# Performance work log

Hardware: AMD Instinct MI355X
Metric: run time of the kernel (lower is better)

The kernel has to match this reference:

```python
import jax, jax.numpy as jnp
import numpy as np

B = 4096       # batch
S = 4096       # seq_len == input_dim
DEPTH = 2
D_MODEL = 1
D_FFN = 2      # d_model * d_ffn_factor
EPS = 1e-5


def _layernorm(x, w, b):
    mu = jnp.mean(x, axis=-1, keepdims=True)
    var = jnp.mean((x - mu) ** 2, axis=-1, keepdims=True)
    return (x - mu) * jax.lax.rsqrt(var + EPS) * w + b


def setup_inputs() -> dict:
    key = jax.random.key(0)
    ks = jax.random.split(key, 16)
    sc = lambda fan_in: 1.0 / np.sqrt(fan_in)
    inp = {
        "x": jax.random.normal(ks[0], (B, S), dtype=jnp.float32),
        # per-depth stacked gMLP block params
        "ln1_w": jnp.ones((DEPTH, D_MODEL), jnp.float32),
        "ln1_b": jnp.zeros((DEPTH, D_MODEL), jnp.float32),
        "cp1_w": jax.random.uniform(ks[1], (DEPTH, D_FFN, D_MODEL), jnp.float32, -sc(D_MODEL), sc(D_MODEL)),
        "cp1_b": jax.random.uniform(ks[2], (DEPTH, D_FFN), jnp.float32, -sc(D_MODEL), sc(D_MODEL)),
        "sgu_ln_w": jnp.ones((DEPTH, D_FFN // 2), jnp.float32),
        "sgu_ln_b": jnp.zeros((DEPTH, D_FFN // 2), jnp.float32),
        "sgu_proj_w": jax.random.uniform(ks[3], (DEPTH, S, S), jnp.float32, -sc(S), sc(S)),
        "sgu_proj_b": jax.random.uniform(ks[4], (DEPTH, S), jnp.float32, -sc(S), sc(S)),
        "cp2_w": jax.random.uniform(ks[5], (DEPTH, D_MODEL, D_FFN // 2), jnp.float32, -sc(D_FFN // 2), sc(D_FFN // 2)),
        "cp2_b": jax.random.uniform(ks[6], (DEPTH, D_MODEL), jnp.float32, -sc(D_FFN // 2), sc(D_FFN // 2)),
        "pooler_w": jax.random.uniform(ks[7], (S, S), jnp.float32, -sc(S), sc(S)),
        "pooler_b": jax.random.uniform(ks[8], (S,), jnp.float32, -sc(S), sc(S)),
        "cls_w": jax.random.uniform(ks[9], (1, S), jnp.float32, -sc(S), sc(S)),
        "cls_b": jax.random.uniform(ks[10], (1,), jnp.float32, -sc(S), sc(S)),
    }
    return inp


def reference(x, ln1_w, ln1_b, cp1_w, cp1_b, sgu_ln_w, sgu_ln_b,
              sgu_proj_w, sgu_proj_b, cp2_w, cp2_b,
              pooler_w, pooler_b, cls_w, cls_b):
    gelu = lambda t: jax.nn.gelu(t, approximate=False)
    h = x[..., None]                                   # [B, S, 1]
    for i in range(DEPTH):
        res = h
        t = _layernorm(h, ln1_w[i], ln1_b[i])          # [B, S, 1]
        t = gelu(t @ cp1_w[i].T + cp1_b[i])            # [B, S, 2]
        u, v = t[..., :D_FFN // 2], t[..., D_FFN // 2:]
        v = _layernorm(v, sgu_ln_w[i], sgu_ln_b[i])
        # transpose(1,2) -> Linear(S,S) -> transpose back, fused as einsum
        v = jnp.einsum('st,btc->bsc', sgu_proj_w[i], v) + sgu_proj_b[i][:, None]
        h = u * v                                      # [B, S, 1]
        h = h @ cp2_w[i].T + cp2_b[i] + res            # [B, S, 1]
    out = h[..., 0]                                    # [B, S]
    out = gelu(out @ pooler_w.T + pooler_b)            # [B, S]
    logits = out @ cls_w.T + cls_b                     # [B, 1]
    return logits[..., 0]                              # [B]
```

## Files before the change

kernel.cpp:

```cpp
#include <hip/hip_runtime.h>


#define K_DIM 4096

typedef __bf16 bf16x8 __attribute__((ext_vector_type(8)));
typedef float f32x4 __attribute__((ext_vector_type(4)));

__device__ __forceinline__ ushort f2bf(float f) {
    unsigned int u = __float_as_uint(f);
    u = (u + 0x7fffu + ((u >> 16) & 1u)) >> 16;
    return (ushort)u;
}

__device__ __forceinline__ float gelu_exact(float x) {
    return 0.5f * x * (1.0f + erff(x * 0.70710678118654752440f));
}

__device__ __forceinline__ void gld16(const void* g, void* l) {
    __builtin_amdgcn_global_load_lds(
        (__attribute__((address_space(1))) void*)(g),
        (__attribute__((address_space(3))) void*)(l), 16, 0, 0);
}

__global__ __launch_bounds__(256) void c_kernel(const float* __restrict__ ln1_b,
                                                const float* __restrict__ cp1_w,
                                                const float* __restrict__ cp1_b,
                                                const float* __restrict__ sgu_ln_b,
                                                const float* __restrict__ sgu_proj_w,
                                                const float* __restrict__ sgu_proj_b,
                                                const float* __restrict__ cp2_w,
                                                const float* __restrict__ cp2_b,
                                                const float* __restrict__ cls_b,
                                                const float* __restrict__ pooler_b,
                                                float* __restrict__ c,
                                                float* __restrict__ e,
                                                float* __restrict__ out) {
    int t = blockIdx.x * 256 + threadIdx.x;
    float cv = 0.0f;
#pragma unroll
    for (int i = 0; i < 2; ++i) {
        float alpha = gelu_exact(ln1_b[i] * cp1_w[i * 2 + 0] + cp1_b[i * 2 + 0]);
        float beta  = sgu_ln_b[i];
        float Ri = 0.0f;
        if (beta != 0.0f) {
            const float* pr = sgu_proj_w + ((size_t)i * 4096 + t) * K_DIM;
            for (int k = 0; k < K_DIM; k += 4) {
                float4 pv = *(const float4*)&pr[k];
                Ri += pv.x + pv.y + pv.z + pv.w;
            }
        }
        float v = beta * Ri + sgu_proj_b[i * 4096 + t];
        cv += alpha * v * cp2_w[i] + cp2_b[i];
    }
    c[t]   = cv;
    e[t]   = pooler_b[t];
    out[t] = cls_b[0];
}

__global__ __launch_bounds__(256) void cvt2_kernel(const float* __restrict__ s0,
                                                   ushort* __restrict__ d0,
                                                   const float* __restrict__ s1,
                                                   ushort* __restrict__ d1,
                                                   const float* __restrict__ c,
                                                   float* __restrict__ e) {
    int b = blockIdx.x;
    bool isP = (b >= 8192);
    const float* src = isP ? s1 : s0;
    ushort* dst = isP ? d1 : d0;
    int i = (b & 8191) * 256 + threadIdx.x;
    const float4* s4 = (const float4*)src + (size_t)i * 2;
    float4 a = s4[0], q = s4[1];
    union { ushort u[8]; uint4 v; } r;
    r.u[0] = f2bf(a.x); r.u[1] = f2bf(a.y); r.u[2] = f2bf(a.z); r.u[3] = f2bf(a.w);
    r.u[4] = f2bf(q.x); r.u[5] = f2bf(q.y); r.u[6] = f2bf(q.z); r.u[7] = f2bf(q.w);
    ((uint4*)dst)[i] = r.v;
    if (isP) {
        int col = (i << 3) & 4095;
        float s = a.x * c[col + 0] + a.y * c[col + 1] + a.z * c[col + 2] + a.w * c[col + 3]
                + q.x * c[col + 4] + q.y * c[col + 5] + q.z * c[col + 6] + q.w * c[col + 7];
#pragma unroll
        for (int m = 1; m < 64; m <<= 1) s += __shfl_xor(s, m);
        if ((threadIdx.x & 63) == 0) atomicAdd(&e[i >> 9], s);
    }
}

__global__ __launch_bounds__(512, 2) void gemm_kernel(const ushort* __restrict__ X,
                                                      const ushort* __restrict__ P,
                                                      const float* __restrict__ clsW,
                                                      const float* __restrict__ e,
                                                      float* __restrict__ accOut) {
    __shared__ __align__(16) ushort As[2][256 * 64];
    __shared__ __align__(16) ushort Bs[2][256 * 64];

    const int t = threadIdx.x;
    const int flat = blockIdx.x;
    const int swz = (flat & 7) * 32 + (flat >> 3);
    const int bRow = swz >> 4, bCol = swz & 15;

    const int lane = t & 63, wv = t >> 6;
    const int g = lane >> 4, lo = lane & 15;
    const int wm = wv >> 2, wn = wv & 3;

    f32x4 zero4 = {0.f, 0.f, 0.f, 0.f};
    f32x4 acc[8][4];
#pragma unroll
    for (int mi = 0; mi < 8; ++mi)
#pragma unroll
        for (int ni = 0; ni < 4; ++ni) acc[mi][ni] = zero4;

    const int sr2 = t >> 3;
    const int cs = (t & 7) ^ (sr2 & 7);
    const ushort* gA = X + (size_t)(bRow * 256 + sr2) * K_DIM + cs * 8;
    const ushort* gB = P + (size_t)(bCol * 256 + sr2) * K_DIM + cs * 8;
    char* lA0 = (char*)&As[0][0] + t * 16;
    char* lB0 = (char*)&Bs[0][0] + t * 16;

#define STAGE_A(buf, h, k0)                                                        \
    do {                                                                           \
        gld16(gA + (size_t)((h) * 128) * K_DIM + (k0), lA0 + (buf) * 32768 + (h) * 16384);      \
        gld16(gA + (size_t)((h) * 128 + 64) * K_DIM + (k0), lA0 + (buf) * 32768 + (h) * 16384 + 8192); \
    } while (0)
#define STAGE_B(buf, h, k0)                                                        \
    do {                                                                           \
        gld16(gB + (size_t)((h) * 128) * K_DIM + (k0), lB0 + (buf) * 32768 + (h) * 16384);      \
        gld16(gB + (size_t)((h) * 128 + 64) * K_DIM + (k0), lB0 + (buf) * 32768 + (h) * 16384 + 8192); \
    } while (0)

#define VMW4 asm volatile("s_waitcnt vmcnt(4)" ::: "memory")
#define VMW0 asm volatile("s_waitcnt vmcnt(0)" ::: "memory")
#define NOSTAGE ((void)0)
#define NOWAIT ((void)0)

#define PHASE(buf, qm, qn, STG, WAIT)                                              \
    do {                                                                           \
        bf16x8 af[4][2], bfr[2][2];                                                \
        _Pragma("unroll") for (int m_ = 0; m_ < 4; ++m_)                           \
            _Pragma("unroll") for (int kk_ = 0; kk_ < 2; ++kk_)                    \
                af[m_][kk_] = *(const bf16x8*)&As[buf][((qm) * 128 + wm * 64 + m_ * 16 + lo) * 64 + ((((kk_ << 2) | g) ^ (lo & 7)) << 3)]; \
        _Pragma("unroll") for (int n_ = 0; n_ < 2; ++n_)                           \
            _Pragma("unroll") for (int kk_ = 0; kk_ < 2; ++kk_)                    \
                bfr[n_][kk_] = *(const bf16x8*)&Bs[buf][((qn) * 128 + wn * 32 + n_ * 16 + lo) * 64 + ((((kk_ << 2) | g) ^ (lo & 7)) << 3)]; \
        STG;                                                                       \
        __builtin_amdgcn_s_barrier();                                              \
        asm volatile("s_waitcnt lgkmcnt(0)" ::: "memory");                         \
        __builtin_amdgcn_sched_barrier(0);                                         \
        __builtin_amdgcn_s_setprio(1);                                             \
        _Pragma("unroll") for (int m_ = 0; m_ < 4; ++m_)                           \
            _Pragma("unroll") for (int n_ = 0; n_ < 2; ++n_)                       \
                _Pragma("unroll") for (int kk_ = 0; kk_ < 2; ++kk_)                \
                    acc[(qm) * 4 + m_][(qn) * 2 + n_] = __builtin_amdgcn_mfma_f32_16x16x32_bf16( \
                        af[m_][kk_], bfr[n_][kk_], acc[(qm) * 4 + m_][(qn) * 2 + n_], 0, 0, 0); \
        __builtin_amdgcn_s_setprio(0);                                             \
        WAIT;                                                                      \
        __builtin_amdgcn_s_barrier();                                              \
    } while (0)

    STAGE_A(0, 0, 0);  STAGE_B(0, 0, 0);
    STAGE_A(0, 1, 0);  STAGE_B(0, 1, 0);
    STAGE_A(1, 0, 64); STAGE_B(1, 0, 64);
    VMW4;
    __builtin_amdgcn_s_barrier();

#pragma unroll 1
    for (int k0 = 0; k0 < 3968; k0 += 128) {
        PHASE(0, 0, 0, STAGE_A(1, 1, k0 + 64),  NOWAIT);
        PHASE(0, 0, 1, STAGE_B(1, 1, k0 + 64),  NOWAIT);
        PHASE(0, 1, 0, STAGE_A(0, 0, k0 + 128), NOWAIT);
        PHASE(0, 1, 1, STAGE_B(0, 0, k0 + 128), VMW4);
        PHASE(1, 0, 0, STAGE_A(0, 1, k0 + 128), NOWAIT);
        PHASE(1, 0, 1, STAGE_B(0, 1, k0 + 128), NOWAIT);
        PHASE(1, 1, 0, STAGE_A(1, 0, k0 + 192), NOWAIT);
        PHASE(1, 1, 1, STAGE_B(1, 0, k0 + 192), VMW4);
    }
    PHASE(0, 0, 0, STAGE_A(1, 1, 4032), NOWAIT);
    PHASE(0, 0, 1, STAGE_B(1, 1, 4032), NOWAIT);
    PHASE(0, 1, 0, NOSTAGE, NOWAIT);
    PHASE(0, 1, 1, NOSTAGE, VMW0);
    PHASE(1, 0, 0, NOSTAGE, NOWAIT);
    PHASE(1, 0, 1, NOSTAGE, NOWAIT);
    PHASE(1, 1, 0, NOSTAGE, NOWAIT);
    PHASE(1, 1, 1, NOSTAGE, NOWAIT);

#undef PHASE
#undef STAGE_A
#undef STAGE_B

    float eb[4], cw[4];
#pragma unroll
    for (int ni = 0; ni < 4; ++ni) {
        int s = bCol * 256 + (ni >> 1) * 128 + wn * 32 + (ni & 1) * 16 + lo;
        eb[ni] = e[s];
        cw[ni] = clsW[s];
    }
#pragma unroll
    for (int mi = 0; mi < 8; ++mi) {
        int rowBase = bRow * 256 + (mi >> 2) * 128 + wm * 64 + (mi & 3) * 16 + g * 4;
#pragma unroll
        for (int r = 0; r < 4; ++r) {
            float sum = 0.0f;
#pragma unroll
            for (int ni = 0; ni < 4; ++ni) {
                float y = acc[mi][ni][r] + eb[ni];
                sum += gelu_exact(y) * cw[ni];
            }
            sum += __shfl_xor(sum, 1);
            sum += __shfl_xor(sum, 2);
            sum += __shfl_xor(sum, 4);
            sum += __shfl_xor(sum, 8);
            if (lo == 0) atomicAdd(&accOut[rowBase + r], sum);
        }
    }
}

extern "C" void kernel_launch(void* const* d_in, const int* in_sizes, int n_in,
                              void* d_out, int out_size, void* d_ws, size_t ws_size,
                              hipStream_t stream) {
    const float* x          = (const float*)d_in[0];
    const float* ln1_b      = (const float*)d_in[2];
    const float* cp1_w      = (const float*)d_in[3];
    const float* cp1_b      = (const float*)d_in[4];
    const float* sgu_ln_b   = (const float*)d_in[6];
    const float* sgu_proj_w = (const float*)d_in[7];
    const float* sgu_proj_b = (const float*)d_in[8];
    const float* cp2_w      = (const float*)d_in[9];
    const float* cp2_b      = (const float*)d_in[10];
    const float* pooler_w   = (const float*)d_in[11];
    const float* pooler_b   = (const float*)d_in[12];
    const float* cls_w      = (const float*)d_in[13];
    const float* cls_b      = (const float*)d_in[14];

    ushort* xb = (ushort*)d_ws;
    ushort* pb = xb + (size_t)K_DIM * K_DIM;
    float*  fs = (float*)(pb + (size_t)K_DIM * K_DIM);
    float* c_buf = fs;
    float* e_buf = fs + 4096;
    float* out   = (float*)d_out;

    c_kernel<<<16, 256, 0, stream>>>(ln1_b, cp1_w, cp1_b, sgu_ln_b, sgu_proj_w,
                                     sgu_proj_b, cp2_w, cp2_b, cls_b, pooler_b,
                                     c_buf, e_buf, out);
    cvt2_kernel<<<16384, 256, 0, stream>>>(x, xb, pooler_w, pb, c_buf, e_buf);
    gemm_kernel<<<256, 512, 0, stream>>>(xb, pb, cls_w, e_buf, out);
}
```

Baseline: 429.8 us.

## Reuse register fragments across GEMM phases and deepen global prefetch

The main GEMM loop now keeps A/B fragments in registers shared across the four quadrant phases, ordered (0,0)->(1,0)->(1,1)->(0,1). Each phase reloads only the operand that changes, which cuts LDS reads per k-step. Global-to-LDS staging is reordered to keep one more stage in flight (vmcnt 6 instead of 4), and the first phase waits with a partial lgkmcnt. This adds register pressure and more complex buffer-hazard reasoning in exchange for less LDS traffic and more load latency hiding.

```diff
diff --git a/kernel.cpp b/kernel.cpp
--- a/kernel.cpp
+++ b/kernel.cpp
@@ -108,6 +108,11 @@
 #pragma unroll
         for (int ni = 0; ni < 4; ++ni) acc[mi][ni] = zero4;
 
+    bf16x8 af[4][2];
+    bf16x8 bfr[2][2];
+    const int ch0 = ((g ^ (lo & 7)) << 3);
+    const int ch1 = (((4 | g) ^ (lo & 7)) << 3);
+
     const int sr2 = t >> 3;
     const int cs = (t & 7) ^ (sr2 & 7);
     const ushort* gA = X + (size_t)(bRow * 256 + sr2) * K_DIM + cs * 8;
@@ -126,62 +131,82 @@
         gld16(gB + (size_t)((h) * 128 + 64) * K_DIM + (k0), lB0 + (buf) * 32768 + (h) * 16384 + 8192); \
     } while (0)
 
-#define VMW4 asm volatile("s_waitcnt vmcnt(4)" ::: "memory")
+#define VMW6 asm volatile("s_waitcnt vmcnt(6)" ::: "memory")
 #define VMW0 asm volatile("s_waitcnt vmcnt(0)" ::: "memory")
 #define NOSTAGE ((void)0)
 #define NOWAIT ((void)0)
-
-#define PHASE(buf, qm, qn, STG, WAIT)                                              \
-    do {                                                                           \
-        bf16x8 af[4][2], bfr[2][2];                                                \
-        _Pragma("unroll") for (int m_ = 0; m_ < 4; ++m_)                           \
-            _Pragma("unroll") for (int kk_ = 0; kk_ < 2; ++kk_)                    \
-                af[m_][kk_] = *(const bf16x8*)&As[buf][((qm) * 128 + wm * 64 + m_ * 16 + lo) * 64 + ((((kk_ << 2) | g) ^ (lo & 7)) << 3)]; \
-        _Pragma("unroll") for (int n_ = 0; n_ < 2; ++n_)                           \
-            _Pragma("unroll") for (int kk_ = 0; kk_ < 2; ++kk_)                    \
-                bfr[n_][kk_] = *(const bf16x8*)&Bs[buf][((qn) * 128 + wn * 32 + n_ * 16 + lo) * 64 + ((((kk_ << 2) | g) ^ (lo & 7)) << 3)]; \
-        STG;                                                                       \
-        __builtin_amdgcn_s_barrier();                                              \
-        asm volatile("s_waitcnt lgkmcnt(0)" ::: "memory");                         \
-        __builtin_amdgcn_sched_barrier(0);                                         \
+#define BAR __builtin_amdgcn_s_barrier()
+#define LGKM0                                                \
+    do {                                                     \
+        asm volatile("s_waitcnt lgkmcnt(0)" ::: "memory");   \
+        __builtin_amdgcn_sched_barrier(0);                   \
+    } while (0)
+
+#define READ_A(buf, qm)                                                            \
+    _Pragma("unroll") for (int m_ = 0; m_ < 4; ++m_) {                             \
+        af[m_][0] = *(const bf16x8*)&As[buf][((qm) * 128 + wm * 64 + m_ * 16 + lo) * 64 + ch0]; \
+        af[m_][1] = *(const bf16x8*)&As[buf][((qm) * 128 + wm * 64 + m_ * 16 + lo) * 64 + ch1]; \
+    }
+#define READ_B(buf, qn)                                                            \
+    _Pragma("unroll") for (int n_ = 0; n_ < 2; ++n_) {                             \
+        bfr[n_][0] = *(const bf16x8*)&Bs[buf][((qn) * 128 + wn * 32 + n_ * 16 + lo) * 64 + ch0]; \
+        bfr[n_][1] = *(const bf16x8*)&Bs[buf][((qn) * 128 + wn * 32 + n_ * 16 + lo) * 64 + ch1]; \
+    }
+#define MFMA16(qm, qn)                                                             \
+    do {                                                                           \
         __builtin_amdgcn_s_setprio(1);                                             \
         _Pragma("unroll") for (int m_ = 0; m_ < 4; ++m_)                           \
-            _Pragma("unroll") for (int n_ = 0; n_ < 2; ++n_)                       \
-                _Pragma("unroll") for (int kk_ = 0; kk_ < 2; ++kk_)                \
-                    acc[(qm) * 4 + m_][(qn) * 2 + n_] = __builtin_amdgcn_mfma_f32_16x16x32_bf16( \
-                        af[m_][kk_], bfr[n_][kk_], acc[(qm) * 4 + m_][(qn) * 2 + n_], 0, 0, 0); \
+            _Pragma("unroll") for (int n_ = 0; n_ < 2; ++n_) {                     \
+                acc[(qm) * 4 + m_][(qn) * 2 + n_] = __builtin_amdgcn_mfma_f32_16x16x32_bf16( \
+                    af[m_][0], bfr[n_][0], acc[(qm) * 4 + m_][(qn) * 2 + n_], 0, 0, 0); \
+                acc[(qm) * 4 + m_][(qn) * 2 + n_] = __builtin_amdgcn_mfma_f32_16x16x32_bf16( \
+                    af[m_][1], bfr[n_][1], acc[(qm) * 4 + m_][(qn) * 2 + n_], 0, 0, 0); \
+            }                                                                      \
         __builtin_amdgcn_s_setprio(0);                                             \
-        WAIT;                                                                      \
-        __builtin_amdgcn_s_barrier();                                              \
-    } while (0)
-
-    STAGE_A(0, 0, 0);  STAGE_B(0, 0, 0);
-    STAGE_A(0, 1, 0);  STAGE_B(0, 1, 0);
-    STAGE_A(1, 0, 64); STAGE_B(1, 0, 64);
-    VMW4;
-    __builtin_amdgcn_s_barrier();
+    } while (0)
+
+#define PH1(b, STG)                                                                \
+    do {                                                                           \
+        READ_A(b, 0); READ_B(b, 0); STG;                                           \
+        asm volatile("s_waitcnt lgkmcnt(8)" ::: "memory");                         \
+        BAR; LGKM0; MFMA16(0, 0); BAR;                                             \
+    } while (0)
+#define PH2(b, STG) do { READ_A(b, 1); STG; BAR; LGKM0; MFMA16(1, 0); BAR; } while (0)
+#define PH3(b, STG) do { READ_B(b, 1); STG; BAR; LGKM0; MFMA16(1, 1); BAR; } while (0)
+#define PH4(b, STG, WAIT) do { READ_A(b, 0); STG; BAR; LGKM0; MFMA16(0, 1); WAIT; BAR; } while (0)
+
+    STAGE_B(0, 0, 0);  STAGE_A(0, 1, 0);  STAGE_B(0, 1, 0);  STAGE_A(0, 0, 0);
+    STAGE_B(1, 0, 64); STAGE_A(1, 1, 64); STAGE_B(1, 1, 64);
+    VMW6;
+    BAR;
 
 #pragma unroll 1
     for (int k0 = 0; k0 < 3968; k0 += 128) {
-        PHASE(0, 0, 0, STAGE_A(1, 1, k0 + 64),  NOWAIT);
-        PHASE(0, 0, 1, STAGE_B(1, 1, k0 + 64),  NOWAIT);
-        PHASE(0, 1, 0, STAGE_A(0, 0, k0 + 128), NOWAIT);
-        PHASE(0, 1, 1, STAGE_B(0, 0, k0 + 128), VMW4);
-        PHASE(1, 0, 0, STAGE_A(0, 1, k0 + 128), NOWAIT);
-        PHASE(1, 0, 1, STAGE_B(0, 1, k0 + 128), NOWAIT);
-        PHASE(1, 1, 0, STAGE_A(1, 0, k0 + 192), NOWAIT);
-        PHASE(1, 1, 1, STAGE_B(1, 0, k0 + 192), VMW4);
-    }
-    PHASE(0, 0, 0, STAGE_A(1, 1, 4032), NOWAIT);
-    PHASE(0, 0, 1, STAGE_B(1, 1, 4032), NOWAIT);
-    PHASE(0, 1, 0, NOSTAGE, NOWAIT);
-    PHASE(0, 1, 1, NOSTAGE, VMW0);
-    PHASE(1, 0, 0, NOSTAGE, NOWAIT);
-    PHASE(1, 0, 1, NOSTAGE, NOWAIT);
-    PHASE(1, 1, 0, NOSTAGE, NOWAIT);
-    PHASE(1, 1, 1, NOSTAGE, NOWAIT);
-
-#undef PHASE
+        PH1(0, STAGE_A(1, 0, k0 + 64));
+        PH2(0, STAGE_B(0, 0, k0 + 128));
+        PH3(0, STAGE_A(0, 1, k0 + 128));
+        PH4(0, STAGE_B(0, 1, k0 + 128), VMW6);
+        PH1(1, STAGE_A(0, 0, k0 + 128));
+        PH2(1, STAGE_B(1, 0, k0 + 192));
+        PH3(1, STAGE_A(1, 1, k0 + 192));
+        PH4(1, STAGE_B(1, 1, k0 + 192), VMW6);
+    }
+    PH1(0, STAGE_A(1, 0, 4032));
+    PH2(0, NOSTAGE);
+    PH3(0, NOSTAGE);
+    PH4(0, NOSTAGE, VMW0);
+    PH1(1, NOSTAGE);
+    PH2(1, NOSTAGE);
+    PH3(1, NOSTAGE);
+    PH4(1, NOSTAGE, NOWAIT);
+
+#undef PH1
+#undef PH2
+#undef PH3
+#undef PH4
+#undef MFMA16
+#undef READ_A
+#undef READ_B
 #undef STAGE_A
 #undef STAGE_B
 
```

Result: faster. 407.7 us (-5.1%).
